# Optimization experiments

Measured on AMD Instinct MI355X. Metric: run time of the kernel, lower is better.

## Reference

```python
import jax, jax.numpy as jnp
import numpy as np

K = 20      # self.k in OurModel
TAU = 1.0   # self.tau in OurModel


def _knn_feats(emb, idx, yctx):
    # emb: [N, E] embedding table; idx: [B] int query ids; yctx: [B, N] residual context
    a = emb[idx]                                            # [B, E] gathered query embeddings
    # squared euclidean via gram trick, then sqrt == torch.cdist(p=2)
    d2 = (jnp.sum(a * a, axis=-1, keepdims=True)
          + jnp.sum(emb * emb, axis=-1)[None, :]
          - 2.0 * a @ emb.T)                                 # [B, N]
    sim = jnp.sqrt(jnp.clip(d2, 0.0, None)) + 0.001
    rows = jnp.arange(idx.shape[0])
    sim = sim.at[rows, idx].set(0.0)                         # zero self-distance
    w = jnp.exp(-sim / TAU)                                  # [B, N], self weight == 1 (max)
    # top (K+1) weights; drop the largest (the self entry) -> top-K neighbours.
    # Matches torch argsort(w)[:, -(K+1):-1]; downstream ops are order-invariant reductions.
    topw, topi = jax.lax.top_k(w, K + 1)
    topw = topw[:, 1:]                                       # [B, K]
    sel = jnp.take_along_axis(yctx, topi[:, 1:], axis=1)     # [B, K]
    f1 = jnp.sum(topw, axis=1)                               # sum of weights
    f2 = jnp.sum(sel * topw, axis=1) / jnp.sum(topw, axis=1) # weighted mean
    f3 = jnp.std(sel, axis=1, ddof=1)                        # torch.std is unbiased
    return f1, f2, f3


def _forward(emb0, emb1, rctx0, rctx1, idx0, idx1, mean_in, std_in,
             W1, b1, Wm, bm, Ws, bs):
    a1, a2, a3 = _knn_feats(emb0, idx0, rctx0)
    b1_, b2_, b3_ = _knn_feats(emb1, idx1, rctx1)
    # torch.cat(final1 + final2 + final3 + [mean, std]) column order
    feats = jnp.stack([a1, b1_, a2, b2_, a3, b3_, mean_in, std_in], axis=1)  # [B, 8]
    h = jnp.maximum(feats @ W1 + b1, 0.0)                    # [B, 64]
    mean_out = h @ Wm + bm[0]                                # [B]
    std_out = h @ Ws + bs[0]                                 # [B]
    return mean_out, std_out


def setup_inputs() -> dict:
    key = jax.random.key(0)
    ks = jax.random.split(key, 14)
    B, N, E, H = 512, 50000, 16, 64
    return {
        "emb0": jax.random.normal(ks[0], (N, E), jnp.float32),
        "emb1": jax.random.normal(ks[1], (N, E), jnp.float32),
        "rctx0": jax.random.normal(ks[2], (B, N), jnp.float32),
        "rctx1": jax.random.normal(ks[3], (B, N), jnp.float32),
        "idx0": jax.random.randint(ks[4], (B,), 0, N, jnp.int32),
        "idx1": jax.random.randint(ks[5], (B,), 0, N, jnp.int32),
        "mean_in": jax.random.normal(ks[6], (B,), jnp.float32),
        "std_in": jax.random.normal(ks[7], (B,), jnp.float32),
        "W1": jax.random.normal(ks[8], (8, H), jnp.float32) * 0.1,
        "b1": jax.random.normal(ks[9], (H,), jnp.float32) * 0.1,
        "Wm": jax.random.normal(ks[10], (H,), jnp.float32) * 0.1,
        "bm": jax.random.normal(ks[11], (1,), jnp.float32) * 0.1,
        "Ws": jax.random.normal(ks[12], (H,), jnp.float32) * 0.1,
        "bs": jax.random.normal(ks[13], (1,), jnp.float32) * 0.1,
    }


def reference(emb0, emb1, rctx0, rctx1, idx0, idx1, mean_in, std_in,
              W1, b1, Wm, bm, Ws, bs):
    return _forward(emb0, emb1, rctx0, rctx1, idx0, idx1, mean_in, std_in,
                    W1, b1, Wm, bm, Ws, bs)
```

## Files before the change

kernel.cpp:

```cpp
#include <hip/hip_runtime.h>
#include <math.h>

typedef unsigned long long u64;
typedef unsigned int u32;
#define INF64 0xFFFFFFFFFFFFFFFFULL
#define FBIG 3.3e38f
#define KSEL 20
#define QT   32
#define CNK  16
#define CAP  256
#define PREFT 4
#define DEPS 0.5f
#define NTHR 512

typedef __bf16 bf16x8 __attribute__((ext_vector_type(8)));
typedef float  f32x16 __attribute__((ext_vector_type(16)));
typedef unsigned int uint4e __attribute__((ext_vector_type(4)));

static __device__ __forceinline__ u32 asu(float f) { return __builtin_bit_cast(u32, f); }
static __device__ __forceinline__ float trunchi(u32 u) { return __builtin_bit_cast(float, u & 0xffff0000u); }
#define PERM2(a,b) __builtin_amdgcn_perm((a),(b),0x07060302u)
static __device__ __forceinline__ bf16x8 mk8(u32 a, u32 b, u32 c, u32 d) {
    uint4e t = {a, b, c, d};
    return __builtin_bit_cast(bf16x8, t);
}
static __device__ __forceinline__ f32x16 zero16() {
    f32x16 z = {0.f,0.f,0.f,0.f,0.f,0.f,0.f,0.f,0.f,0.f,0.f,0.f,0.f,0.f,0.f,0.f};
    return z;
}

static __device__ __forceinline__ float dot16(
    float4 a0, float4 a1, float4 a2, float4 a3,
    float4 b0, float4 b1, float4 b2, float4 b3)
{
    float d = 0.f;
    d = fmaf(a0.x, b0.x, d); d = fmaf(a0.y, b0.y, d);
    d = fmaf(a0.z, b0.z, d); d = fmaf(a0.w, b0.w, d);
    d = fmaf(a1.x, b1.x, d); d = fmaf(a1.y, b1.y, d);
    d = fmaf(a1.z, b1.z, d); d = fmaf(a1.w, b1.w, d);
    d = fmaf(a2.x, b2.x, d); d = fmaf(a2.y, b2.y, d);
    d = fmaf(a2.z, b2.z, d); d = fmaf(a2.w, b2.w, d);
    d = fmaf(a3.x, b3.x, d); d = fmaf(a3.y, b3.y, d);
    d = fmaf(a3.z, b3.z, d); d = fmaf(a3.w, b3.w, d);
    return d;
}

static __device__ __forceinline__ void cvt_hilo(float4 f0, float4 f1, bf16x8& hi, bf16x8& lo) {
    u32 u0=asu(f0.x),u1=asu(f0.y),u2=asu(f0.z),u3=asu(f0.w);
    u32 u4=asu(f1.x),u5=asu(f1.y),u6=asu(f1.z),u7=asu(f1.w);
    hi = mk8(PERM2(u1,u0), PERM2(u3,u2), PERM2(u5,u4), PERM2(u7,u6));
    u32 w0=asu(f0.x-trunchi(u0)), w1=asu(f0.y-trunchi(u1));
    u32 w2=asu(f0.z-trunchi(u2)), w3=asu(f0.w-trunchi(u3));
    u32 w4=asu(f1.x-trunchi(u4)), w5=asu(f1.y-trunchi(u5));
    u32 w6=asu(f1.z-trunchi(u6)), w7=asu(f1.w-trunchi(u7));
    lo = mk8(PERM2(w1,w0), PERM2(w3,w2), PERM2(w5,w4), PERM2(w7,w6));
}

static __device__ __forceinline__ f32x16 tile_qe(
    const float* __restrict__ embS, int base, int col, int kb, int N,
    bf16x8 B1, bf16x8 B2)
{
    int row = base + col;
    row = min(row, N - 1);
    const float4* ep = (const float4*)(embS + (size_t)row * 16 + kb * 8);
    float4 f0 = ep[0], f1 = ep[1];
    bf16x8 A1, A2;
    cvt_hilo(f0, f1, A1, A2);
    f32x16 acc = zero16();
    acc = __builtin_amdgcn_mfma_f32_32x32x16_bf16(A1, B1, acc, 0, 0, 0);
    acc = __builtin_amdgcn_mfma_f32_32x32x16_bf16(A1, B2, acc, 0, 0, 0);
    acc = __builtin_amdgcn_mfma_f32_32x32x16_bf16(A2, B1, acc, 0, 0, 0);
    return acc;
}

__global__ __launch_bounds__(256) void norm_kernel(
    const float* __restrict__ emb0, const float* __restrict__ emb1,
    float* __restrict__ neBuf, int N, int npad)
{
    const int j = blockIdx.x * 256 + threadIdx.x;
    const float* __restrict__ e = blockIdx.y ? emb1 : emb0;
    float* __restrict__ o = neBuf + (size_t)blockIdx.y * npad;
    float v = FBIG;
    if (j < N) {
        const float4* p = (const float4*)(e + (size_t)j * 16);
        float4 e0=p[0],e1=p[1],e2=p[2],e3=p[3];
        v = dot16(e0,e1,e2,e3, e0,e1,e2,e3);
    }
    if (j < npad) o[j] = v;
}

__global__ __launch_bounds__(NTHR, 4) void knn_scan_kernel(
    const float* __restrict__ emb0, const float* __restrict__ emb1,
    const int* __restrict__ idx0, const int* __restrict__ idx1,
    const float* __restrict__ neBuf,
    u64* __restrict__ chunkTop, int N, int B, int chlen)
{
    const int tid  = threadIdx.x;
    const int lane = tid & 63;
    const int wv   = tid >> 6;
    const int col  = lane & 31;
    const int kb   = lane >> 5;
    const int bx   = blockIdx.x;
    const int xcd  = bx & 7;
    const int s    = xcd & 1;
    const int t_   = (bx >> 3) * 4 + (xcd >> 1);
    const int c    = t_ & (CNK - 1);
    const int qt   = t_ >> 4;
    const int qbase = qt * QT;
    const int jbeg = c * chlen;
    const int tpc  = chlen >> 5;
    const int npad = chlen * CNK;

    const float* __restrict__ embS = s ? emb1 : emb0;
    const int*   __restrict__ idxp = s ? idx1 : idx0;
    const float* __restrict__ neS  = neBuf + (size_t)s * npad;

    __shared__ float Qs[QT][16];
    __shared__ float naS[QT];
    __shared__ int   sq[QT];
    __shared__ int   scnt[QT];
    __shared__ float sthr[QT];
    __shared__ float sMin[QT][32];
    __shared__ u32   sbuf[QT][CAP];

    if (tid < QT) { sq[tid] = idxp[qbase + tid]; scnt[tid] = 0; }
    __syncthreads();
    if (tid < 128) {
        int q = tid >> 2, part = tid & 3;
        ((float4*)(&Qs[q][0]))[part] = ((const float4*)(embS + (size_t)sq[q] * 16))[part];
    }
    __syncthreads();
    if (tid < QT) {
        const float4* qp = (const float4*)(&Qs[tid][0]);
        float4 a0=qp[0],a1=qp[1],a2=qp[2],a3=qp[3];
        naS[tid] = dot16(a0,a1,a2,a3, a0,a1,a2,a3);
    }
    bf16x8 B1, B2;
    {
        const float4* qp = (const float4*)(&Qs[col][kb * 8]);
        float4 f0 = qp[0], f1 = qp[1];
        cvt_hilo(f0, f1, B1, B2);
    }
    __syncthreads();

    const float na_l  = naS[col];
    const int   self_l = sq[col];

    float m0v = FBIG, m1v = FBIG;
#define PINS(r, nef) { float v_ = fmaf(acc[r], -2.f, na_l + (nef)); \
    float t1_ = fminf(m1v, fmaxf(m0v, v_)); m0v = fminf(m0v, v_); m1v = t1_; }
    for (int pt = 0; pt < PREFT; ++pt) {
        const int t = wv + pt * 8;
        const int base = jbeg + t * 32;
        const float4* np_ = (const float4*)(neS + base + kb * 4);
        float4 n0 = np_[0], n1 = np_[2], n2 = np_[4], n3 = np_[6];
        f32x16 acc = tile_qe(embS, base, col, kb, N, B1, B2);
        PINS(0,n0.x)  PINS(1,n0.y)  PINS(2,n0.z)  PINS(3,n0.w)
        PINS(4,n1.x)  PINS(5,n1.y)  PINS(6,n1.z)  PINS(7,n1.w)
        PINS(8,n2.x)  PINS(9,n2.y)  PINS(10,n2.z) PINS(11,n2.w)
        PINS(12,n3.x) PINS(13,n3.y) PINS(14,n3.z) PINS(15,n3.w)
    }
#undef PINS
    sMin[col][(wv * 2 + kb) * 2 + 0] = fmaxf(m0v, 0.f);
    sMin[col][(wv * 2 + kb) * 2 + 1] = fmaxf(m1v, 0.f);
    __syncthreads();

    for (int qq = 0; qq < 4; ++qq) {
        const int q = wv * 4 + qq;
        const u32 vb = (lane < 32) ? asu(sMin[q][lane]) : 0xFFFFFFFFu;
        u32 T = 0;
        for (int bb = 30; bb >= 0; --bb) {
            u32 U = T | ((1u << bb) - 1u);
            int nle = __popcll(__ballot(vb <= U));
            if (nle < KSEL + 1) T |= (1u << bb);
        }
        if (lane == 0) sthr[q] = __uint_as_float(T) + DEPS;
    }
    __syncthreads();
    const float thr_l = sthr[col];

#define EPI(r, nef) { float ad_ = fmaf(acc[r], -2.f, na_l + (nef)); \
    if (ad_ <= thr_l) msk |= (1u << (r)); }
    for (int t = wv; t < tpc; t += 8) {
        const int base = jbeg + t * 32;
        const float4* np_ = (const float4*)(neS + base + kb * 4);
        float4 n0 = np_[0], n1 = np_[2], n2 = np_[4], n3 = np_[6];
        f32x16 acc = tile_qe(embS, base, col, kb, N, B1, B2);
        u32 msk = 0;
        EPI(0,n0.x)  EPI(1,n0.y)  EPI(2,n0.z)  EPI(3,n0.w)
        EPI(4,n1.x)  EPI(5,n1.y)  EPI(6,n1.z)  EPI(7,n1.w)
        EPI(8,n2.x)  EPI(9,n2.y)  EPI(10,n2.z) EPI(11,n2.w)
        EPI(12,n3.x) EPI(13,n3.y) EPI(14,n3.z) EPI(15,n3.w)
        while (msk) {
            int r = __ffs(msk) - 1;
            msk &= msk - 1;
            int j = base + (r & 3) + 8 * (r >> 2) + 4 * kb;
            if (j != self_l) {
                int sl = atomicAdd(&scnt[col], 1);
                if (sl < CAP) sbuf[col][sl] = (u32)j;
            }
        }
    }
#undef EPI
    __syncthreads();

    for (int qq = 0; qq < 4; ++qq) {
        const int q = wv * 4 + qq;
        const int M = min(scnt[q], CAP);
        const float4* qp = (const float4*)(&Qs[q][0]);
        const float4 q0=qp[0], q1=qp[1], q2=qp[2], q3=qp[3];
        const float naq = naS[q];
        auto rk = [&](int i) -> u64 {
            int j = (int)sbuf[q][i];
            const float4* p = (const float4*)(embS + (size_t)j * 16);
            float4 e0=p[0],e1=p[1],e2=p[2],e3=p[3];
            float qe  = dot16(q0,q1,q2,q3, e0,e1,e2,e3);
            float dd  = fmaxf(fmaf(qe, -2.f, naq + neS[j]), 0.f);
            return ((u64)asu(dd) << 32) | (u32)j;
        };
        u64 k0 = (lane < M)       ? rk(lane)       : INF64;
        u64 k1 = (lane + 64 < M)  ? rk(lane + 64)  : INF64;
        u64 k2 = (lane + 128 < M) ? rk(lane + 128) : INF64;
        u64 k3 = (lane + 192 < M) ? rk(lane + 192) : INF64;
        u64 T = 0;
        for (int bb = 63; bb >= 32; --bb) {
            u64 U = T | ((1ull << bb) - 1ull);
            int nle = __popcll(__ballot(k0 <= U)) + __popcll(__ballot(k1 <= U))
                    + __popcll(__ballot(k2 <= U)) + __popcll(__ballot(k3 <= U));
            if (nle < KSEL) T |= (1ull << bb);
        }
        for (int bb = 15; bb >= 0; --bb) {
            u64 U = T | ((1ull << bb) - 1ull);
            int nle = __popcll(__ballot(k0 <= U)) + __popcll(__ballot(k1 <= U))
                    + __popcll(__ballot(k2 <= U)) + __popcll(__ballot(k3 <= U));
            if (nle < KSEL) T |= (1ull << bb);
        }
        u64* dst = chunkTop + ((size_t)(s * B + qbase + q) * CNK + c) * KSEL;
        int basec = 0;
        {
            u64 mm = __ballot(k0 <= T);
            if (k0 <= T) { int sl = basec + __popcll(mm & ((1ull << lane) - 1ull)); if (sl < KSEL) dst[sl] = k0; }
            basec += __popcll(mm);
        }
        {
            u64 mm = __ballot(k1 <= T);
            if (k1 <= T) { int sl = basec + __popcll(mm & ((1ull << lane) - 1ull)); if (sl < KSEL) dst[sl] = k1; }
            basec += __popcll(mm);
        }
        {
            u64 mm = __ballot(k2 <= T);
            if (k2 <= T) { int sl = basec + __popcll(mm & ((1ull << lane) - 1ull)); if (sl < KSEL) dst[sl] = k2; }
            basec += __popcll(mm);
        }
        {
            u64 mm = __ballot(k3 <= T);
            if (k3 <= T) { int sl = basec + __popcll(mm & ((1ull << lane) - 1ull)); if (sl < KSEL) dst[sl] = k3; }
            basec += __popcll(mm);
        }
        for (int sl = basec + lane; sl < KSEL; sl += 64) dst[sl] = INF64;
    }
}

__global__ __launch_bounds__(128) void merge_mlp_kernel(
    const u64* __restrict__ chunkTop,
    const float* __restrict__ rctx0, const float* __restrict__ rctx1,
    const float* __restrict__ mean_in, const float* __restrict__ std_in,
    const float* __restrict__ W1, const float* __restrict__ b1,
    const float* __restrict__ Wm, const float* __restrict__ bm,
    const float* __restrict__ Ws, const float* __restrict__ bs,
    float* __restrict__ out, int N, int B)
{
    const int b = blockIdx.x;
    const int tid = threadIdx.x;
    const int s = tid >> 6;
    const int lane = tid & 63;
    __shared__ float sf[8];

    const u64* src = chunkTop + ((size_t)(s * B + b)) * (CNK * KSEL);
    u64 v0 = src[lane];
    u64 v1 = src[lane + 64];
    u64 v2 = src[lane + 128];
    u64 v3 = src[lane + 192];
    u64 v4 = src[lane + 256];
    u64 T = 0;
    for (int bb = 63; bb >= 32; --bb) {
        u64 U = T | ((1ull << bb) - 1ull);
        int nle = __popcll(__ballot(v0 <= U)) + __popcll(__ballot(v1 <= U))
                + __popcll(__ballot(v2 <= U)) + __popcll(__ballot(v3 <= U))
                + __popcll(__ballot(v4 <= U));
        if (nle < KSEL) T |= (1ull << bb);
    }
    for (int bb = 15; bb >= 0; --bb) {
        u64 U = T | ((1ull << bb) - 1ull);
        int nle = __popcll(__ballot(v0 <= U)) + __popcll(__ballot(v1 <= U))
                + __popcll(__ballot(v2 <= U)) + __popcll(__ballot(v3 <= U))
                + __popcll(__ballot(v4 <= U));
        if (nle < KSEL) T |= (1ull << bb);
    }
    const float* __restrict__ rctx = s ? rctx1 : rctx0;
    float sw = 0.f, ssw = 0.f, ss = 0.f, ss2 = 0.f;
#define ACC(vx) if (vx <= T && vx != INF64) { \
        float d2 = __uint_as_float((u32)((vx) >> 32)); \
        int j = (int)(u32)((vx) & 0xFFFFFFFFULL); \
        float sim = sqrtf(d2) + 0.001f; \
        float wr = expf(-sim); \
        float svr = rctx[(size_t)b * N + j]; \
        sw += wr; ssw += svr * wr; ss += svr; ss2 += svr * svr; }
    ACC(v0) ACC(v1) ACC(v2) ACC(v3) ACC(v4)
#undef ACC
#pragma unroll
    for (int o = 32; o; o >>= 1) {
        sw  += __shfl_down(sw,  o, 64);
        ssw += __shfl_down(ssw, o, 64);
        ss  += __shfl_down(ss,  o, 64);
        ss2 += __shfl_down(ss2, o, 64);
    }
    if (lane == 0) {
        sf[0 + s] = sw;
        sf[2 + s] = ssw / sw;
        float mean = ss * (1.f / KSEL);
        float var = (ss2 - (float)KSEL * mean * mean) * (1.f / (KSEL - 1));
        sf[4 + s] = sqrtf(fmaxf(var, 0.f));
        if (s == 0) { sf[6] = mean_in[b]; sf[7] = std_in[b]; }
    }
    __syncthreads();

    if (tid < 64) {
        float f0 = sf[0], f1 = sf[1], f2 = sf[2], f3 = sf[3];
        float f4 = sf[4], f5 = sf[5], f6 = sf[6], f7 = sf[7];
        float h = b1[lane];
        h = fmaf(f0, W1[0 * 64 + lane], h);
        h = fmaf(f1, W1[1 * 64 + lane], h);
        h = fmaf(f2, W1[2 * 64 + lane], h);
        h = fmaf(f3, W1[3 * 64 + lane], h);
        h = fmaf(f4, W1[4 * 64 + lane], h);
        h = fmaf(f5, W1[5 * 64 + lane], h);
        h = fmaf(f6, W1[6 * 64 + lane], h);
        h = fmaf(f7, W1[7 * 64 + lane], h);
        h = fmaxf(h, 0.f);
        float mo = h * Wm[lane], so = h * Ws[lane];
#pragma unroll
        for (int o = 32; o; o >>= 1) {
            mo += __shfl_down(mo, o, 64);
            so += __shfl_down(so, o, 64);
        }
        if (lane == 0) {
            out[b] = mo + bm[0];
            out[B + b] = so + bs[0];
        }
    }
}

extern "C" void kernel_launch(void* const* d_in, const int* in_sizes, int n_in,
                              void* d_out, int out_size, void* d_ws, size_t ws_size,
                              hipStream_t stream) {
    const float* emb0    = (const float*)d_in[0];
    const float* emb1    = (const float*)d_in[1];
    const float* rctx0   = (const float*)d_in[2];
    const float* rctx1   = (const float*)d_in[3];
    const int*   idx0    = (const int*)d_in[4];
    const int*   idx1    = (const int*)d_in[5];
    const float* mean_in = (const float*)d_in[6];
    const float* std_in  = (const float*)d_in[7];
    const float* W1      = (const float*)d_in[8];
    const float* b1      = (const float*)d_in[9];
    const float* Wm      = (const float*)d_in[10];
    const float* bm      = (const float*)d_in[11];
    const float* Ws      = (const float*)d_in[12];
    const float* bs      = (const float*)d_in[13];

    const int B = in_sizes[4];
    const int N = in_sizes[0] / 16;

    int chlen = (((N + CNK - 1) / CNK) + 31) & ~31;
    int npad  = chlen * CNK;

    float* neBuf = (float*)d_ws;
    u64* chunkTop = (u64*)((char*)d_ws + (size_t)2 * npad * sizeof(float));

    norm_kernel<<<dim3(npad / 256, 2), 256, 0, stream>>>(emb0, emb1, neBuf, N, npad);

    knn_scan_kernel<<<dim3(2 * (B / QT) * CNK), NTHR, 0, stream>>>(
        emb0, emb1, idx0, idx1, neBuf, chunkTop, N, B, chlen);

    merge_mlp_kernel<<<dim3(B), 128, 0, stream>>>(
        chunkTop, rctx0, rctx1, mean_in, std_in,
        W1, b1, Wm, bm, Ws, bs, (float*)d_out, N, B);
}
```

Measured before the change: 259.5 us.

## Double chunk count, raise occupancy, and shortcut radix-select in refine/merge

Measured after the change: 281.6 us. 1.08x slower.

```diff
diff --git a/kernel.cpp b/kernel.cpp
--- a/kernel.cpp
+++ b/kernel.cpp
@@ -7,9 +7,10 @@
 #define FBIG 3.3e38f
 #define KSEL 20
 #define QT   32
-#define CNK  16
+#define CNK  32
+#define CNKSH 5
 #define CAP  256
-#define PREFT 4
+#define PREFT 2
 #define DEPS 0.5f
 #define NTHR 512
 
@@ -89,7 +90,113 @@
     if (j < npad) o[j] = v;
 }
 
-__global__ __launch_bounds__(NTHR, 4) void knn_scan_kernel(
+__device__ __attribute__((noinline)) float bound21(const float* sMinq, int lane) {
+    const u32 vb = (lane < 32) ? asu(sMinq[lane]) : 0xFFFFFFFFu;
+    u32 T = 0;
+#pragma unroll 1
+    for (int bb = 30; bb >= 16; --bb) {
+        u32 U = T | ((1u << bb) - 1u);
+        int nle = __popcll(__ballot(vb <= U));
+        if (nle < KSEL + 1) T |= (1u << bb);
+    }
+    return __uint_as_float(T | 0xFFFFu) + DEPS;
+}
+
+__device__ __attribute__((noinline)) void refine_q(
+    const float* __restrict__ embS, const float* __restrict__ neS,
+    const u32* __restrict__ sbufq, const float4* qp, float naq,
+    int M, u64* __restrict__ dst, int lane)
+{
+    const float4 q0 = qp[0], q1 = qp[1], q2 = qp[2], q3 = qp[3];
+    auto rk = [&](int i) -> u64 {
+        int j = (int)sbufq[i];
+        const float4* p = (const float4*)(embS + (size_t)j * 16);
+        float4 e0 = p[0], e1 = p[1], e2 = p[2], e3 = p[3];
+        float qe = dot16(q0, q1, q2, q3, e0, e1, e2, e3);
+        float dd = fmaxf(fmaf(qe, -2.f, naq + neS[j]), 0.f);
+        return ((u64)asu(dd) << 32) | (u32)j;
+    };
+    u64 k0 = (lane < M) ? rk(lane) : INF64;
+    if (M <= 64) {
+        u64 T = 0;
+#pragma unroll 1
+        for (int bb = 62; bb >= 32; --bb) {
+            u64 U = T | ((1ull << bb) - 1ull);
+            int nle = __popcll(__ballot(k0 <= U));
+            if (nle < KSEL) T |= (1ull << bb);
+        }
+        {
+            u64 U = T | 0xFFFFull;
+            int m = __popcll(__ballot(k0 <= U));
+            if (m == KSEL) T = U;
+            else {
+#pragma unroll 1
+                for (int bb = 15; bb >= 0; --bb) {
+                    u64 U2 = T | ((1ull << bb) - 1ull);
+                    int nle = __popcll(__ballot(k0 <= U2));
+                    if (nle < KSEL) T |= (1ull << bb);
+                }
+            }
+        }
+        u64 mm = __ballot(k0 <= T);
+        if (k0 <= T) {
+            int sl = __popcll(mm & ((1ull << lane) - 1ull));
+            if (sl < KSEL) dst[sl] = k0;
+        }
+        for (int sl = __popcll(mm) + lane; sl < KSEL; sl += 64) dst[sl] = INF64;
+    } else {
+        u64 k1 = (lane + 64 < M)  ? rk(lane + 64)  : INF64;
+        u64 k2 = (lane + 128 < M) ? rk(lane + 128) : INF64;
+        u64 k3 = (lane + 192 < M) ? rk(lane + 192) : INF64;
+        u64 T = 0;
+#pragma unroll 1
+        for (int bb = 62; bb >= 32; --bb) {
+            u64 U = T | ((1ull << bb) - 1ull);
+            int nle = __popcll(__ballot(k0 <= U)) + __popcll(__ballot(k1 <= U))
+                    + __popcll(__ballot(k2 <= U)) + __popcll(__ballot(k3 <= U));
+            if (nle < KSEL) T |= (1ull << bb);
+        }
+        {
+            u64 U = T | 0xFFFFull;
+            int m = __popcll(__ballot(k0 <= U)) + __popcll(__ballot(k1 <= U))
+                  + __popcll(__ballot(k2 <= U)) + __popcll(__ballot(k3 <= U));
+            if (m == KSEL) T = U;
+            else {
+#pragma unroll 1
+                for (int bb = 15; bb >= 0; --bb) {
+                    u64 U2 = T | ((1ull << bb) - 1ull);
+                    int nle = __popcll(__ballot(k0 <= U2)) + __popcll(__ballot(k1 <= U2))
+                            + __popcll(__ballot(k2 <= U2)) + __popcll(__ballot(k3 <= U2));
+                    if (nle < KSEL) T |= (1ull << bb);
+                }
+            }
+        }
+        int basec = 0;
+        {
+            u64 mm = __ballot(k0 <= T);
+            if (k0 <= T) { int sl = basec + __popcll(mm & ((1ull << lane) - 1ull)); if (sl < KSEL) dst[sl] = k0; }
+            basec += __popcll(mm);
+        }
+        {
+            u64 mm = __ballot(k1 <= T);
+            if (k1 <= T) { int sl = basec + __popcll(mm & ((1ull << lane) - 1ull)); if (sl < KSEL) dst[sl] = k1; }
+            basec += __popcll(mm);
+        }
+        {
+            u64 mm = __ballot(k2 <= T);
+            if (k2 <= T) { int sl = basec + __popcll(mm & ((1ull << lane) - 1ull)); if (sl < KSEL) dst[sl] = k2; }
+            basec += __popcll(mm);
+        }
+        {
+            u64 mm = __ballot(k3 <= T);
+            if (k3 <= T) { int sl = basec + __popcll(mm & ((1ull << lane) - 1ull)); if (sl < KSEL) dst[sl] = k3; }
+            basec += __popcll(mm);
+        }
+        for (int sl = basec + lane; sl < KSEL; sl += 64) dst[sl] = INF64;
+    }
+}
+
+__global__ __launch_bounds__(NTHR, 8) void knn_scan_kernel(
     const float* __restrict__ emb0, const float* __restrict__ emb1,
     const int* __restrict__ idx0, const int* __restrict__ idx1,
     const float* __restrict__ neBuf,
@@ -105,7 +212,7 @@
     const int s    = xcd & 1;
     const int t_   = (bx >> 3) * 4 + (xcd >> 1);
     const int c    = t_ & (CNK - 1);
-    const int qt   = t_ >> 4;
+    const int qt   = t_ >> CNKSH;
     const int qbase = qt * QT;
     const int jbeg = c * chlen;
     const int tpc  = chlen >> 5;
@@ -120,7 +227,7 @@
     __shared__ int   sq[QT];
     __shared__ int   scnt[QT];
     __shared__ float sthr[QT];
-    __shared__ float sMin[QT][32];
+    __shared__ float sMin[QT][33];
     __shared__ u32   sbuf[QT][CAP];
 
     if (tid < QT) { sq[tid] = idxp[qbase + tid]; scnt[tid] = 0; }
@@ -167,14 +274,8 @@
 
     for (int qq = 0; qq < 4; ++qq) {
         const int q = wv * 4 + qq;
-        const u32 vb = (lane < 32) ? asu(sMin[q][lane]) : 0xFFFFFFFFu;
-        u32 T = 0;
-        for (int bb = 30; bb >= 0; --bb) {
-            u32 U = T | ((1u << bb) - 1u);
-            int nle = __popcll(__ballot(vb <= U));
-            if (nle < KSEL + 1) T |= (1u << bb);
-        }
-        if (lane == 0) sthr[q] = __uint_as_float(T) + DEPS;
+        float thr = bound21(&sMin[q][0], lane);
+        if (lane == 0) sthr[q] = thr;
     }
     __syncthreads();
     const float thr_l = sthr[col];
@@ -206,58 +307,9 @@
 
     for (int qq = 0; qq < 4; ++qq) {
         const int q = wv * 4 + qq;
-        const int M = min(scnt[q], CAP);
-        const float4* qp = (const float4*)(&Qs[q][0]);
-        const float4 q0=qp[0], q1=qp[1], q2=qp[2], q3=qp[3];
-        const float naq = naS[q];
-        auto rk = [&](int i) -> u64 {
-            int j = (int)sbuf[q][i];
-            const float4* p = (const float4*)(embS + (size_t)j * 16);
-            float4 e0=p[0],e1=p[1],e2=p[2],e3=p[3];
-            float qe  = dot16(q0,q1,q2,q3, e0,e1,e2,e3);
-            float dd  = fmaxf(fmaf(qe, -2.f, naq + neS[j]), 0.f);
-            return ((u64)asu(dd) << 32) | (u32)j;
-        };
-        u64 k0 = (lane < M)       ? rk(lane)       : INF64;
-        u64 k1 = (lane + 64 < M)  ? rk(lane + 64)  : INF64;
-        u64 k2 = (lane + 128 < M) ? rk(lane + 128) : INF64;
-        u64 k3 = (lane + 192 < M) ? rk(lane + 192) : INF64;
-        u64 T = 0;
-        for (int bb = 63; bb >= 32; --bb) {
-            u64 U = T | ((1ull << bb) - 1ull);
-            int nle = __popcll(__ballot(k0 <= U)) + __popcll(__ballot(k1 <= U))
-                    + __popcll(__ballot(k2 <= U)) + __popcll(__ballot(k3 <= U));
-            if (nle < KSEL) T |= (1ull << bb);
-        }
-        for (int bb = 15; bb >= 0; --bb) {
-            u64 U = T | ((1ull << bb) - 1ull);
-            int nle = __popcll(__ballot(k0 <= U)) + __popcll(__ballot(k1 <= U))
-                    + __popcll(__ballot(k2 <= U)) + __popcll(__ballot(k3 <= U));
-            if (nle < KSEL) T |= (1ull << bb);
-        }
         u64* dst = chunkTop + ((size_t)(s * B + qbase + q) * CNK + c) * KSEL;
-        int basec = 0;
-        {
-            u64 mm = __ballot(k0 <= T);
-            if (k0 <= T) { int sl = basec + __popcll(mm & ((1ull << lane) - 1ull)); if (sl < KSEL) dst[sl] = k0; }
-            basec += __popcll(mm);
-        }
-        {
-            u64 mm = __ballot(k1 <= T);
-            if (k1 <= T) { int sl = basec + __popcll(mm & ((1ull << lane) - 1ull)); if (sl < KSEL) dst[sl] = k1; }
-            basec += __popcll(mm);
-        }
-        {
-            u64 mm = __ballot(k2 <= T);
-            if (k2 <= T) { int sl = basec + __popcll(mm & ((1ull << lane) - 1ull)); if (sl < KSEL) dst[sl] = k2; }
-            basec += __popcll(mm);
-        }
-        {
-            u64 mm = __ballot(k3 <= T);
-            if (k3 <= T) { int sl = basec + __popcll(mm & ((1ull << lane) - 1ull)); if (sl < KSEL) dst[sl] = k3; }
-            basec += __popcll(mm);
-        }
-        for (int sl = basec + lane; sl < KSEL; sl += 64) dst[sl] = INF64;
+        refine_q(embS, neS, &sbuf[q][0], (const float4*)(&Qs[q][0]), naS[q],
+                 min(scnt[q], CAP), dst, lane);
     }
 }
 
@@ -282,24 +334,40 @@
     u64 v2 = src[lane + 128];
     u64 v3 = src[lane + 192];
     u64 v4 = src[lane + 256];
+    u64 v5 = src[lane + 320];
+    u64 v6 = src[lane + 384];
+    u64 v7 = src[lane + 448];
+    u64 v8 = src[lane + 512];
+    u64 v9 = src[lane + 576];
+#define NLE(U) (__popcll(__ballot(v0 <= (U))) + __popcll(__ballot(v1 <= (U))) \
+              + __popcll(__ballot(v2 <= (U))) + __popcll(__ballot(v3 <= (U))) \
+              + __popcll(__ballot(v4 <= (U))) + __popcll(__ballot(v5 <= (U))) \
+              + __popcll(__ballot(v6 <= (U))) + __popcll(__ballot(v7 <= (U))) \
+              + __popcll(__ballot(v8 <= (U))) + __popcll(__ballot(v9 <= (U))))
     u64 T = 0;
-    for (int bb = 63; bb >= 32; --bb) {
+#pragma unroll 1
+    for (int bb = 62; bb >= 32; --bb) {
         u64 U = T | ((1ull << bb) - 1ull);
-        int nle = __popcll(__ballot(v0 <= U)) + __popcll(__ballot(v1 <= U))
-                + __popcll(__ballot(v2 <= U)) + __popcll(__ballot(v3 <= U))
-                + __popcll(__ballot(v4 <= U));
+        int nle = NLE(U);
         if (nle < KSEL) T |= (1ull << bb);
     }
-    for (int bb = 15; bb >= 0; --bb) {
-        u64 U = T | ((1ull << bb) - 1ull);
-        int nle = __popcll(__ballot(v0 <= U)) + __popcll(__ballot(v1 <= U))
-                + __popcll(__ballot(v2 <= U)) + __popcll(__ballot(v3 <= U))
-                + __popcll(__ballot(v4 <= U));
-        if (nle < KSEL) T |= (1ull << bb);
-    }
+    {
+        u64 U = T | 0xFFFFull;
+        int m = NLE(U);
+        if (m == KSEL) T = U;
+        else {
+#pragma unroll 1
+            for (int bb = 15; bb >= 0; --bb) {
+                u64 U2 = T | ((1ull << bb) - 1ull);
+                int nle = NLE(U2);
+                if (nle < KSEL) T |= (1ull << bb);
+            }
+        }
+    }
+#undef NLE
     const float* __restrict__ rctx = s ? rctx1 : rctx0;
     float sw = 0.f, ssw = 0.f, ss = 0.f, ss2 = 0.f;
-#define ACC(vx) if (vx <= T && vx != INF64) { \
+#define ACC(vx) if ((vx) <= T) { \
         float d2 = __uint_as_float((u32)((vx) >> 32)); \
         int j = (int)(u32)((vx) & 0xFFFFFFFFULL); \
         float sim = sqrtf(d2) + 0.001f; \
@@ -307,6 +375,7 @@
         float svr = rctx[(size_t)b * N + j]; \
         sw += wr; ssw += svr * wr; ss += svr; ss2 += svr * svr; }
     ACC(v0) ACC(v1) ACC(v2) ACC(v3) ACC(v4)
+    ACC(v5) ACC(v6) ACC(v7) ACC(v8) ACC(v9)
 #undef ACC
 #pragma unroll
     for (int o = 32; o; o >>= 1) {
```
